# Kernel tuning notes

Hardware: AMD Instinct MI355X
Metric: run time of the kernel (lower is better)

Reference implementation:

```python
import jax, jax.numpy as jnp
import numpy as np

HEADS = 8
DIM_HEAD = 32
SCALE = DIM_HEAD ** -0.5


def setup_inputs() -> dict:
    key = jax.random.key(0)
    k1, k2, k3 = jax.random.split(key, 3)
    B, H, W, C = 16, 64, 64, 256
    hidden = HEADS * DIM_HEAD  # 256
    x = jax.random.normal(k1, (B, H, W, C), dtype=jnp.float32)
    # 1x1 convs with no bias == dense matmuls over channel dim (glorot-ish scale)
    w_qkv = jax.random.normal(k2, (C, 3 * hidden), dtype=jnp.float32) * (1.0 / np.sqrt(C))
    w_out = jax.random.normal(k3, (hidden, C), dtype=jnp.float32) * (1.0 / np.sqrt(hidden))
    return {"x": x, "w_qkv": w_qkv, "w_out": w_out}


def reference(x, w_qkv, w_out):
    B, H, W, C = x.shape
    n = H * W
    # to_qkv: 1x1 conv, no bias
    qkv = jnp.einsum('bhwc,cf->bhwf', x, w_qkv)  # [B,H,W,3*hidden]
    q, k, v = jnp.split(qkv, 3, axis=-1)

    def to_heads(t):
        # 'b x y (h c) -> b h c (x y)'
        t = t.reshape(B, n, HEADS, DIM_HEAD)
        return jnp.transpose(t, (0, 2, 3, 1))  # [B, heads, dim_head, n]

    q, k, v = to_heads(q), to_heads(k), to_heads(v)
    q = jax.nn.softmax(q, axis=-2) * SCALE      # softmax over feature dim d
    k = jax.nn.softmax(k, axis=-1)              # softmax over spatial dim n
    context = jnp.einsum('bhdn,bhen->bhde', k, v)   # [B, heads, d, e]
    out = jnp.einsum('bhde,bhdn->bhen', context, q)  # [B, heads, e, n]
    # 'b h c (x y) -> b x y (h c)'
    out = jnp.transpose(out, (0, 3, 1, 2)).reshape(B, H, W, HEADS * DIM_HEAD)
    # to_out: 1x1 conv, no bias
    return jnp.einsum('bhwf,fc->bhwc', out, w_out)
```

## Files before the change

### kernel.cpp

```cpp
#include <hip/hip_runtime.h>

using short8 = __attribute__((ext_vector_type(8))) short;
using f32x4  = __attribute__((ext_vector_type(4))) float;

#define SCALE_Q 0.17677669529663687f
#define NCHUNK 16

__device__ __forceinline__ unsigned short f2bf(float f) {
  unsigned u = __float_as_uint(f);
  return (unsigned short)((u + 0x7FFFu + ((u >> 16) & 1u)) >> 16);
}
__device__ __forceinline__ float bf2f(unsigned h) { return __uint_as_float(h << 16); }

__device__ __forceinline__ void bf8_to_f(uint4 r, float* o) {
  o[0] = bf2f(r.x & 0xffffu); o[1] = bf2f(r.x >> 16);
  o[2] = bf2f(r.y & 0xffffu); o[3] = bf2f(r.y >> 16);
  o[4] = bf2f(r.z & 0xffffu); o[5] = bf2f(r.z >> 16);
  o[6] = bf2f(r.w & 0xffffu); o[7] = bf2f(r.w >> 16);
}

__global__ __launch_bounds__(256) void prep_kernel(
    const float* __restrict__ x, const float* __restrict__ wqkv, const float* __restrict__ wout,
    unsigned short* __restrict__ xb, unsigned short* __restrict__ wqkvT,
    unsigned short* __restrict__ woutT) {
  const int blk = blockIdx.x;
  if (blk < 16384) {
    const size_t i = ((size_t)blk * 256 + threadIdx.x) * 4;
    const float4 v = *(const float4*)(x + i);
    *(ushort4*)(xb + i) = make_ushort4(f2bf(v.x), f2bf(v.y), f2bf(v.z), f2bf(v.w));
  } else if (blk < 16384 + 768) {
    const int n = blk - 16384, k = threadIdx.x;
    wqkvT[n * 256 + k] = f2bf(wqkv[(size_t)k * 768 + n]);
  } else {
    const int c = blk - 16384 - 768, f = threadIdx.x;
    woutT[c * 256 + f] = f2bf(wout[(size_t)f * 256 + c]);
  }
}

template <typename OutT, bool QSOFT, bool SWZ>
__global__ __launch_bounds__(256) void gemm_bt(
    const unsigned short* __restrict__ A, const unsigned short* __restrict__ BT,
    OutT* __restrict__ D, unsigned short* __restrict__ QS,
    int nbn, int K,
    size_t strideA, size_t strideB, size_t strideD) {
  __shared__ unsigned short As[128][40];
  __shared__ unsigned short Bs[128][40];
  int bn, bm;
  if (SWZ) {
    const int cpx = gridDim.x >> 3;
    const int lin = ((int)blockIdx.x & 7) * cpx + ((int)blockIdx.x >> 3);
    bn = lin % nbn; bm = lin / nbn;
  } else {
    bn = blockIdx.x; bm = blockIdx.y;
  }
  const int bz = blockIdx.z;
  const int tid = threadIdx.x, lane = tid & 63, wid = tid >> 6;
  const int wr = wid >> 1, wc = wid & 1;
  const int fr = lane & 15, hi = lane >> 4, fk = hi * 8;
  f32x4 acc[4][4] = {};
  const size_t abase = (size_t)bz * strideA + (size_t)bm * 128 * K;
  const size_t bbase = (size_t)bz * strideB + (size_t)bn * 128 * K;

  for (int kt = 0; kt < K; kt += 32) {
    for (int c = tid; c < 512; c += 256) {
      const int row = c >> 2, kc = (c & 3) * 8;
      *(uint4*)&As[row][kc] = *(const uint4*)(A + abase + (size_t)row * K + kt + kc);
      *(uint4*)&Bs[row][kc] = *(const uint4*)(BT + bbase + (size_t)row * K + kt + kc);
    }
    __syncthreads();
    short8 af[4], bfv[4];
#pragma unroll
    for (int i = 0; i < 4; ++i) {
      af[i]  = *(const short8*)&As[wr * 64 + i * 16 + fr][fk];
      bfv[i] = *(const short8*)&Bs[wc * 64 + i * 16 + fr][fk];
    }
#pragma unroll
    for (int mi = 0; mi < 4; ++mi)
#pragma unroll
      for (int nj = 0; nj < 4; ++nj)
        acc[mi][nj] = __builtin_amdgcn_mfma_f32_16x16x32_bf16(bfv[nj], af[mi], acc[mi][nj], 0, 0, 0);
    __syncthreads();
  }

  const size_t r0 = (size_t)bm * 128 + wr * 64;
  if (QSOFT && bn < 2) {
    const int c0 = bn * 128 + wc * 64;
#pragma unroll
    for (int mi = 0; mi < 4; ++mi) {
      const size_t row = r0 + mi * 16 + fr;
#pragma unroll
      for (int p = 0; p < 2; ++p) {
        const f32x4 a0 = acc[mi][2 * p], a1 = acc[mi][2 * p + 1];
        float mx = fmaxf(fmaxf(fmaxf(a0[0], a0[1]), fmaxf(a0[2], a0[3])),
                         fmaxf(fmaxf(a1[0], a1[1]), fmaxf(a1[2], a1[3])));
        mx = fmaxf(mx, __shfl_xor(mx, 16, 64));
        mx = fmaxf(mx, __shfl_xor(mx, 32, 64));
        float e0[4], e1[4], s = 0.f;
#pragma unroll
        for (int r = 0; r < 4; ++r) {
          e0[r] = __expf(a0[r] - mx); e1[r] = __expf(a1[r] - mx);
          s += e0[r] + e1[r];
        }
        s += __shfl_xor(s, 16, 64);
        s += __shfl_xor(s, 32, 64);
        const float inv = SCALE_Q / s;
        unsigned short* qp = QS + row * 256 + c0 + p * 32 + hi * 4;
        *(ushort4*)(qp)      = make_ushort4(f2bf(e0[0]*inv), f2bf(e0[1]*inv), f2bf(e0[2]*inv), f2bf(e0[3]*inv));
        *(ushort4*)(qp + 16) = make_ushort4(f2bf(e1[0]*inv), f2bf(e1[1]*inv), f2bf(e1[2]*inv), f2bf(e1[3]*inv));
      }
    }
    return;
  }
  const int colbase = (QSOFT ? (bn - 2) : bn) * 128 + wc * 64;
  const int ncols = QSOFT ? 512 : 256;
  OutT* Dz = D + (size_t)bz * strideD;
#pragma unroll
  for (int mi = 0; mi < 4; ++mi) {
    const size_t row = r0 + mi * 16 + fr;
#pragma unroll
    for (int nj = 0; nj < 4; ++nj) {
      const int col0 = colbase + nj * 16 + hi * 4;
      const f32x4 v = acc[mi][nj];
      if constexpr (sizeof(OutT) == 2) {
        *(ushort4*)((unsigned short*)Dz + row * ncols + col0) =
            make_ushort4(f2bf(v[0]), f2bf(v[1]), f2bf(v[2]), f2bf(v[3]));
      } else {
        *(float4*)((float*)Dz + row * ncols + col0) = make_float4(v[0], v[1], v[2], v[3]);
      }
    }
  }
}

__global__ __launch_bounds__(256) void ctx_part_kernel(const unsigned short* __restrict__ kv,
                                                       float* __restrict__ part,
                                                       float* __restrict__ spart) {
  const int blk = blockIdx.x;
  const int bh = blk >> 4, chunk = blk & 15;
  const int b = bh >> 3, h = bh & 7;
  const int tid = threadIdx.x, d = tid & 31, g = tid >> 5;
  const unsigned short* kbase =
      kv + (size_t)b * 4096 * 512 + h * 32 + (size_t)chunk * 256 * 512;
  const unsigned short* vbase = kbase + 256;

  __shared__ float ek[64][36], vv[64][36];
  float a0 = 0.f, a1 = 0.f, a2 = 0.f, a3 = 0.f, ssum = 0.f;
  const int e0 = g * 4;
  const int sn = tid >> 2, sc = (tid & 3) * 8;
  const unsigned short* kp0 = kbase + (size_t)sn * 512 + sc;
  const unsigned short* vp0 = vbase + (size_t)sn * 512 + sc;
  uint4 kr = *(const uint4*)kp0;
  uint4 vr = *(const uint4*)vp0;
  for (int n0 = 0; n0 < 256; n0 += 64) {
    float kf[8], vf[8];
    bf8_to_f(kr, kf); bf8_to_f(vr, vf);
    uint4 krn = kr, vrn = vr;
    if (n0 + 64 < 256) {
      krn = *(const uint4*)(kp0 + (size_t)(n0 + 64) * 512);
      vrn = *(const uint4*)(vp0 + (size_t)(n0 + 64) * 512);
    }
#pragma unroll
    for (int j = 0; j < 8; ++j) { ek[sn][sc + j] = __expf(kf[j]); vv[sn][sc + j] = vf[j]; }
    __syncthreads();
#pragma unroll 8
    for (int i = 0; i < 64; ++i) {
      const float kd = ek[i][d];
      const float4 v4 = *(const float4*)&vv[i][e0];
      ssum += kd;
      a0 += kd * v4.x; a1 += kd * v4.y; a2 += kd * v4.z; a3 += kd * v4.w;
    }
    __syncthreads();
    kr = krn; vr = vrn;
  }
  float* pp = part + ((size_t)chunk * 128 + bh) * 1024 + d * 32 + e0;
  pp[0] = a0; pp[1] = a1; pp[2] = a2; pp[3] = a3;
  if (g == 0) spart[((size_t)chunk * 128 + bh) * 32 + d] = ssum;
}

__global__ __launch_bounds__(256) void ctx_combine_kernel(const float* __restrict__ part,
                                                          const float* __restrict__ spart,
                                                          float* __restrict__ ctx) {
  const int bh = blockIdx.x, tid = threadIdx.x;
  __shared__ float sinv[32];
  if (tid < 32) {
    float s = 0.f;
#pragma unroll
    for (int c = 0; c < NCHUNK; ++c) s += spart[((size_t)c * 128 + bh) * 32 + tid];
    sinv[tid] = 1.0f / s;
  }
  __syncthreads();
  float4 acc = make_float4(0.f, 0.f, 0.f, 0.f);
#pragma unroll
  for (int c = 0; c < NCHUNK; ++c) {
    const float4 p = *(const float4*)(part + ((size_t)c * 128 + bh) * 1024 + tid * 4);
    acc.x += p.x; acc.y += p.y; acc.z += p.z; acc.w += p.w;
  }
  const float si = sinv[tid >> 3];
  float4* cp = (float4*)(ctx + (size_t)bh * 1024 + tid * 4);
  *cp = make_float4(acc.x * si, acc.y * si, acc.z * si, acc.w * si);
}

__global__ __launch_bounds__(256) void w2_kernel(const float* __restrict__ ctx,
                                                 const unsigned short* __restrict__ woutT,
                                                 unsigned short* __restrict__ W2T) {
  const int b = blockIdx.x >> 4, cg = blockIdx.x & 15;
  const int tid = threadIdx.x;
  __shared__ float cs[8 * 32 * 32];
  {
    const float4* src = (const float4*)(ctx + (size_t)b * 8192);
    float4* dst = (float4*)cs;
#pragma unroll
    for (int i = 0; i < 8; ++i) dst[tid + i * 256] = src[tid + i * 256];
  }
  __syncthreads();
  const int c = cg * 16 + (tid >> 4), chunk = tid & 15;
  const int h = chunk >> 1, d0 = (chunk & 1) * 16;
  float wf[32];
  {
    const uint4* wp = (const uint4*)(woutT + (size_t)c * 256 + h * 32);
    bf8_to_f(wp[0], wf + 0); bf8_to_f(wp[1], wf + 8);
    bf8_to_f(wp[2], wf + 16); bf8_to_f(wp[3], wf + 24);
  }
  unsigned short o[16];
#pragma unroll
  for (int dd = 0; dd < 16; ++dd) {
    const float* cp = cs + h * 1024 + (d0 + dd) * 32;
    float acc = 0.f;
#pragma unroll
    for (int e = 0; e < 32; ++e) acc += cp[e] * wf[e];
    o[dd] = f2bf(acc);
  }
  uint4* op = (uint4*)(W2T + ((size_t)b * 256 + c) * 256 + chunk * 16);
  op[0] = make_uint4((unsigned)o[0] | ((unsigned)o[1] << 16), (unsigned)o[2] | ((unsigned)o[3] << 16),
                     (unsigned)o[4] | ((unsigned)o[5] << 16), (unsigned)o[6] | ((unsigned)o[7] << 16));
  op[1] = make_uint4((unsigned)o[8] | ((unsigned)o[9] << 16), (unsigned)o[10] | ((unsigned)o[11] << 16),
                     (unsigned)o[12] | ((unsigned)o[13] << 16), (unsigned)o[14] | ((unsigned)o[15] << 16));
}

extern "C" void kernel_launch(void* const* d_in, const int* in_sizes, int n_in,
                              void* d_out, int out_size, void* d_ws, size_t ws_size,
                              hipStream_t stream) {
  const float* x     = (const float*)d_in[0];
  const float* wqkv  = (const float*)d_in[1];
  const float* wout  = (const float*)d_in[2];
  float* out = (float*)d_out;

  char* ws = (char*)d_ws;
  unsigned short* xb    = (unsigned short*)(ws);
  unsigned short* wqkvT = (unsigned short*)(ws + 33554432);
  unsigned short* woutT = (unsigned short*)(ws + 33947648);
  unsigned short* kv    = (unsigned short*)(ws + 34078720);
  float*          ctx   = (float*)        (ws + 101187584);
  unsigned short* qs    = (unsigned short*)(ws + 101711872);
  float*          part  = (float*)(ws);
  float*          spart = (float*)(ws + 8388608);
  unsigned short* W2T   = (unsigned short*)(ws + 12582912);

  prep_kernel<<<16384 + 768 + 256, 256, 0, stream>>>(x, wqkv, wout, xb, wqkvT, woutT);
  gemm_bt<unsigned short, true, true><<<3072, 256, 0, stream>>>(
      xb, wqkvT, kv, qs, 6, 256, 0, 0, 0);
  ctx_part_kernel<<<2048, 256, 0, stream>>>(kv, part, spart);
  ctx_combine_kernel<<<128, 256, 0, stream>>>(part, spart, ctx);
  w2_kernel<<<256, 256, 0, stream>>>(ctx, woutT, W2T);
  gemm_bt<float, false, false><<<dim3(2, 32, 16), 256, 0, stream>>>(
      qs, W2T, out, nullptr, 2, 256,
      (size_t)4096 * 256, (size_t)256 * 256, (size_t)4096 * 256);
}
```

Baseline: 166.8 us.

## Fuse fp32-to-bf16 conversion of x into QKV GEMM with register-resident B tiles

Drops the separate pass that converts x to bf16; the QKV GEMM now reads fp32 x directly and converts to bf16 while staging into shared memory. The GEMM is restructured to a 64x128 tile, with each wave keeping its full K=256 slice of B in registers and A double-buffered in LDS with a prefetch of the next stage. The aim is to avoid writing and re-reading a 32MB bf16 copy of x and to overlap global loads with MFMA work. In exchange the kernel holds more registers per thread (occupancy hint of 3 blocks) and launches twice as many blocks, each loading B from global memory.

Result: slower. 185.8 us (+11.4%).

```diff
diff --git a/kernel.cpp b/kernel.cpp
--- a/kernel.cpp
+++ b/kernel.cpp
@@ -11,6 +11,9 @@
   return (unsigned short)((u + 0x7FFFu + ((u >> 16) & 1u)) >> 16);
 }
 __device__ __forceinline__ float bf2f(unsigned h) { return __uint_as_float(h << 16); }
+__device__ __forceinline__ unsigned pack2(float a, float b) {
+  return (unsigned)f2bf(a) | ((unsigned)f2bf(b) << 16);
+}
 
 __device__ __forceinline__ void bf8_to_f(uint4 r, float* o) {
   o[0] = bf2f(r.x & 0xffffu); o[1] = bf2f(r.x >> 16);
@@ -20,105 +23,129 @@
 }
 
 __global__ __launch_bounds__(256) void prep_kernel(
-    const float* __restrict__ x, const float* __restrict__ wqkv, const float* __restrict__ wout,
-    unsigned short* __restrict__ xb, unsigned short* __restrict__ wqkvT,
-    unsigned short* __restrict__ woutT) {
+    const float* __restrict__ wqkv, const float* __restrict__ wout,
+    unsigned short* __restrict__ wqkvT, unsigned short* __restrict__ woutT) {
   const int blk = blockIdx.x;
-  if (blk < 16384) {
-    const size_t i = ((size_t)blk * 256 + threadIdx.x) * 4;
-    const float4 v = *(const float4*)(x + i);
-    *(ushort4*)(xb + i) = make_ushort4(f2bf(v.x), f2bf(v.y), f2bf(v.z), f2bf(v.w));
-  } else if (blk < 16384 + 768) {
-    const int n = blk - 16384, k = threadIdx.x;
+  if (blk < 768) {
+    const int n = blk, k = threadIdx.x;
     wqkvT[n * 256 + k] = f2bf(wqkv[(size_t)k * 768 + n]);
   } else {
-    const int c = blk - 16384 - 768, f = threadIdx.x;
+    const int c = blk - 768, f = threadIdx.x;
     woutT[c * 256 + f] = f2bf(wout[(size_t)f * 256 + c]);
   }
 }
 
-template <typename OutT, bool QSOFT, bool SWZ>
-__global__ __launch_bounds__(256) void gemm_bt(
-    const unsigned short* __restrict__ A, const unsigned short* __restrict__ BT,
+template <typename InT, typename OutT, bool QSOFT, bool SWZ>
+__global__ __launch_bounds__(256, 3) void gemm_fused(
+    const InT* __restrict__ A, const unsigned short* __restrict__ BT,
     OutT* __restrict__ D, unsigned short* __restrict__ QS,
-    int nbn, int K,
-    size_t strideA, size_t strideB, size_t strideD) {
-  __shared__ unsigned short As[128][40];
-  __shared__ unsigned short Bs[128][40];
+    int nbn, size_t strideA, size_t strideB, size_t strideD) {
+  __shared__ unsigned short As[2][64][72];
   int bn, bm;
   if (SWZ) {
     const int cpx = gridDim.x >> 3;
     const int lin = ((int)blockIdx.x & 7) * cpx + ((int)blockIdx.x >> 3);
     bn = lin % nbn; bm = lin / nbn;
   } else {
-    bn = blockIdx.x; bm = blockIdx.y;
-  }
-  const int bz = blockIdx.z;
+    bn = blockIdx.x % nbn; bm = blockIdx.x / nbn;
+  }
+  const int z = blockIdx.z;
   const int tid = threadIdx.x, lane = tid & 63, wid = tid >> 6;
-  const int wr = wid >> 1, wc = wid & 1;
-  const int fr = lane & 15, hi = lane >> 4, fk = hi * 8;
-  f32x4 acc[4][4] = {};
-  const size_t abase = (size_t)bz * strideA + (size_t)bm * 128 * K;
-  const size_t bbase = (size_t)bz * strideB + (size_t)bn * 128 * K;
-
-  for (int kt = 0; kt < K; kt += 32) {
-    for (int c = tid; c < 512; c += 256) {
-      const int row = c >> 2, kc = (c & 3) * 8;
-      *(uint4*)&As[row][kc] = *(const uint4*)(A + abase + (size_t)row * K + kt + kc);
-      *(uint4*)&Bs[row][kc] = *(const uint4*)(BT + bbase + (size_t)row * K + kt + kc);
-    }
+  const int fr = lane & 15, hi = lane >> 4;
+
+  short8 bfv[2][8];
+  {
+    const unsigned short* Bb =
+        BT + (size_t)z * strideB + ((size_t)bn * 128 + wid * 32 + fr) * 256 + hi * 8;
+#pragma unroll
+    for (int nj = 0; nj < 2; ++nj)
+#pragma unroll
+      for (int kk = 0; kk < 8; ++kk)
+        bfv[nj][kk] = *(const short8*)(Bb + (size_t)nj * 16 * 256 + kk * 32);
+  }
+
+  const int srow = tid >> 2, sk = (tid & 3) * 16;
+  const size_t arow = (size_t)bm * 64 + srow;
+
+  float4 f0, f1, f2, f3; uint4 q0, q1;
+  auto load_stage = [&](int kt) {
+    if constexpr (sizeof(InT) == 4) {
+      const float4* Ag = (const float4*)((const float*)A + (size_t)z * strideA + arow * 256 + kt + sk);
+      f0 = Ag[0]; f1 = Ag[1]; f2 = Ag[2]; f3 = Ag[3];
+    } else {
+      const unsigned short* Ag = (const unsigned short*)A + (size_t)z * strideA + arow * 256 + kt + sk;
+      q0 = *(const uint4*)Ag; q1 = *(const uint4*)(Ag + 8);
+    }
+  };
+  auto write_stage = [&](int buf) {
+    uint4 lo, hi4;
+    if constexpr (sizeof(InT) == 4) {
+      lo  = make_uint4(pack2(f0.x, f0.y), pack2(f0.z, f0.w), pack2(f1.x, f1.y), pack2(f1.z, f1.w));
+      hi4 = make_uint4(pack2(f2.x, f2.y), pack2(f2.z, f2.w), pack2(f3.x, f3.y), pack2(f3.z, f3.w));
+    } else { lo = q0; hi4 = q1; }
+    *(uint4*)&As[buf][srow][sk]     = lo;
+    *(uint4*)&As[buf][srow][sk + 8] = hi4;
+  };
+
+  f32x4 acc[4][2] = {};
+  load_stage(0); write_stage(0);
+  __syncthreads();
+  int cur = 0;
+#pragma unroll
+  for (int t = 0; t < 4; ++t) {
+    if (t < 3) load_stage((t + 1) * 64);
+#pragma unroll
+    for (int kk = 0; kk < 2; ++kk) {
+      short8 af[4];
+#pragma unroll
+      for (int mi = 0; mi < 4; ++mi)
+        af[mi] = *(const short8*)&As[cur][mi * 16 + fr][kk * 32 + hi * 8];
+#pragma unroll
+      for (int mi = 0; mi < 4; ++mi)
+#pragma unroll
+        for (int nj = 0; nj < 2; ++nj)
+          acc[mi][nj] = __builtin_amdgcn_mfma_f32_16x16x32_bf16(
+              bfv[nj][t * 2 + kk], af[mi], acc[mi][nj], 0, 0, 0);
+    }
+    if (t < 3) write_stage(cur ^ 1);
     __syncthreads();
-    short8 af[4], bfv[4];
-#pragma unroll
-    for (int i = 0; i < 4; ++i) {
-      af[i]  = *(const short8*)&As[wr * 64 + i * 16 + fr][fk];
-      bfv[i] = *(const short8*)&Bs[wc * 64 + i * 16 + fr][fk];
-    }
-#pragma unroll
-    for (int mi = 0; mi < 4; ++mi)
-#pragma unroll
-      for (int nj = 0; nj < 4; ++nj)
-        acc[mi][nj] = __builtin_amdgcn_mfma_f32_16x16x32_bf16(bfv[nj], af[mi], acc[mi][nj], 0, 0, 0);
-    __syncthreads();
-  }
-
-  const size_t r0 = (size_t)bm * 128 + wr * 64;
+    cur ^= 1;
+  }
+
+  const size_t r0 = (size_t)bm * 64;
   if (QSOFT && bn < 2) {
-    const int c0 = bn * 128 + wc * 64;
+    const int c0 = bn * 128 + wid * 32;
 #pragma unroll
     for (int mi = 0; mi < 4; ++mi) {
       const size_t row = r0 + mi * 16 + fr;
-#pragma unroll
-      for (int p = 0; p < 2; ++p) {
-        const f32x4 a0 = acc[mi][2 * p], a1 = acc[mi][2 * p + 1];
-        float mx = fmaxf(fmaxf(fmaxf(a0[0], a0[1]), fmaxf(a0[2], a0[3])),
-                         fmaxf(fmaxf(a1[0], a1[1]), fmaxf(a1[2], a1[3])));
-        mx = fmaxf(mx, __shfl_xor(mx, 16, 64));
-        mx = fmaxf(mx, __shfl_xor(mx, 32, 64));
-        float e0[4], e1[4], s = 0.f;
-#pragma unroll
-        for (int r = 0; r < 4; ++r) {
-          e0[r] = __expf(a0[r] - mx); e1[r] = __expf(a1[r] - mx);
-          s += e0[r] + e1[r];
-        }
-        s += __shfl_xor(s, 16, 64);
-        s += __shfl_xor(s, 32, 64);
-        const float inv = SCALE_Q / s;
-        unsigned short* qp = QS + row * 256 + c0 + p * 32 + hi * 4;
-        *(ushort4*)(qp)      = make_ushort4(f2bf(e0[0]*inv), f2bf(e0[1]*inv), f2bf(e0[2]*inv), f2bf(e0[3]*inv));
-        *(ushort4*)(qp + 16) = make_ushort4(f2bf(e1[0]*inv), f2bf(e1[1]*inv), f2bf(e1[2]*inv), f2bf(e1[3]*inv));
+      const f32x4 a0 = acc[mi][0], a1 = acc[mi][1];
+      float mx = fmaxf(fmaxf(fmaxf(a0[0], a0[1]), fmaxf(a0[2], a0[3])),
+                       fmaxf(fmaxf(a1[0], a1[1]), fmaxf(a1[2], a1[3])));
+      mx = fmaxf(mx, __shfl_xor(mx, 16, 64));
+      mx = fmaxf(mx, __shfl_xor(mx, 32, 64));
+      float e0[4], e1[4], s = 0.f;
+#pragma unroll
+      for (int r = 0; r < 4; ++r) {
+        e0[r] = __expf(a0[r] - mx); e1[r] = __expf(a1[r] - mx);
+        s += e0[r] + e1[r];
       }
+      s += __shfl_xor(s, 16, 64);
+      s += __shfl_xor(s, 32, 64);
+      const float inv = SCALE_Q / s;
+      unsigned short* qp = QS + row * 256 + c0 + hi * 4;
+      *(ushort4*)(qp)      = make_ushort4(f2bf(e0[0]*inv), f2bf(e0[1]*inv), f2bf(e0[2]*inv), f2bf(e0[3]*inv));
+      *(ushort4*)(qp + 16) = make_ushort4(f2bf(e1[0]*inv), f2bf(e1[1]*inv), f2bf(e1[2]*inv), f2bf(e1[3]*inv));
     }
     return;
   }
-  const int colbase = (QSOFT ? (bn - 2) : bn) * 128 + wc * 64;
+  const int colbase = (QSOFT ? (bn - 2) * 128 : bn * 128) + wid * 32;
   const int ncols = QSOFT ? 512 : 256;
-  OutT* Dz = D + (size_t)bz * strideD;
+  OutT* Dz = D + (size_t)z * strideD;
 #pragma unroll
   for (int mi = 0; mi < 4; ++mi) {
     const size_t row = r0 + mi * 16 + fr;
 #pragma unroll
-    for (int nj = 0; nj < 4; ++nj) {
+    for (int nj = 0; nj < 2; ++nj) {
       const int col0 = colbase + nj * 16 + hi * 4;
       const f32x4 v = acc[mi][nj];
       if constexpr (sizeof(OutT) == 2) {
@@ -245,23 +272,21 @@
   float* out = (float*)d_out;
 
   char* ws = (char*)d_ws;
-  unsigned short* xb    = (unsigned short*)(ws);
+  float*          part  = (float*)(ws);
+  float*          spart = (float*)(ws + 8388608);
+  unsigned short* W2T   = (unsigned short*)(ws + 12582912);
   unsigned short* wqkvT = (unsigned short*)(ws + 33554432);
   unsigned short* woutT = (unsigned short*)(ws + 33947648);
   unsigned short* kv    = (unsigned short*)(ws + 34078720);
   float*          ctx   = (float*)        (ws + 101187584);
   unsigned short* qs    = (unsigned short*)(ws + 101711872);
-  float*          part  = (float*)(ws);
-  float*          spart = (float*)(ws + 8388608);
-  unsigned short* W2T   = (unsigned short*)(ws + 12582912);
-
-  prep_kernel<<<16384 + 768 + 256, 256, 0, stream>>>(x, wqkv, wout, xb, wqkvT, woutT);
-  gemm_bt<unsigned short, true, true><<<3072, 256, 0, stream>>>(
-      xb, wqkvT, kv, qs, 6, 256, 0, 0, 0);
+
+  prep_kernel<<<1024, 256, 0, stream>>>(wqkv, wout, wqkvT, woutT);
+  gemm_fused<float, unsigned short, true, true><<<6144, 256, 0, stream>>>(
+      x, wqkvT, kv, qs, 6, 0, 0, 0);
   ctx_part_kernel<<<2048, 256, 0, stream>>>(kv, part, spart);
   ctx_combine_kernel<<<128, 256, 0, stream>>>(part, spart, ctx);
   w2_kernel<<<256, 256, 0, stream>>>(ctx, woutT, W2T);
-  gemm_bt<float, false, false><<<dim3(2, 32, 16), 256, 0, stream>>>(
-      qs, W2T, out, nullptr, 2, 256,
-      (size_t)4096 * 256, (size_t)256 * 256, (size_t)4096 * 256);
-}
+  gemm_fused<unsigned short, float, false, false><<<dim3(128, 1, 16), 256, 0, stream>>>(
+      qs, W2T, out, nullptr, 2, (size_t)4096 * 256, (size_t)256 * 256, (size_t)4096 * 256);
+}
```

## Fuse x bf16 conversion into QKV GEMM load and exp(k) into epilogue

Applied to the files above, without the earlier changes.

The QKV GEMM now reads fp32 x directly and converts it to bf16 while staging into shared memory. This drops the separate pass that wrote a bf16 copy of x. The exponential of k moves from ctx_part_kernel into the GEMM epilogue for the k columns, and the XCD-aware block swizzle is replaced by a plain 2D grid. The GEMM now reads twice the A bytes per tile and may lose L2 locality without the swizzle; exp(k) is stored in bf16 rather than computed in fp32.

Result: slower. 181.5 us (+8.8%).

```diff
diff --git a/kernel.cpp b/kernel.cpp
--- a/kernel.cpp
+++ b/kernel.cpp
@@ -11,6 +11,9 @@
   return (unsigned short)((u + 0x7FFFu + ((u >> 16) & 1u)) >> 16);
 }
 __device__ __forceinline__ float bf2f(unsigned h) { return __uint_as_float(h << 16); }
+__device__ __forceinline__ unsigned pack2(float a, float b) {
+  return (unsigned)f2bf(a) | ((unsigned)f2bf(b) << 16);
+}
 
 __device__ __forceinline__ void bf8_to_f(uint4 r, float* o) {
   o[0] = bf2f(r.x & 0xffffu); o[1] = bf2f(r.x >> 16);
@@ -20,40 +23,26 @@
 }
 
 __global__ __launch_bounds__(256) void prep_kernel(
-    const float* __restrict__ x, const float* __restrict__ wqkv, const float* __restrict__ wout,
-    unsigned short* __restrict__ xb, unsigned short* __restrict__ wqkvT,
-    unsigned short* __restrict__ woutT) {
+    const float* __restrict__ wqkv, const float* __restrict__ wout,
+    unsigned short* __restrict__ wqkvT, unsigned short* __restrict__ woutT) {
   const int blk = blockIdx.x;
-  if (blk < 16384) {
-    const size_t i = ((size_t)blk * 256 + threadIdx.x) * 4;
-    const float4 v = *(const float4*)(x + i);
-    *(ushort4*)(xb + i) = make_ushort4(f2bf(v.x), f2bf(v.y), f2bf(v.z), f2bf(v.w));
-  } else if (blk < 16384 + 768) {
-    const int n = blk - 16384, k = threadIdx.x;
+  if (blk < 768) {
+    const int n = blk, k = threadIdx.x;
     wqkvT[n * 256 + k] = f2bf(wqkv[(size_t)k * 768 + n]);
   } else {
-    const int c = blk - 16384 - 768, f = threadIdx.x;
+    const int c = blk - 768, f = threadIdx.x;
     woutT[c * 256 + f] = f2bf(wout[(size_t)f * 256 + c]);
   }
 }
 
-template <typename OutT, bool QSOFT, bool SWZ>
+template <typename InT, typename OutT, bool QSOFT>
 __global__ __launch_bounds__(256) void gemm_bt(
-    const unsigned short* __restrict__ A, const unsigned short* __restrict__ BT,
+    const InT* __restrict__ A, const unsigned short* __restrict__ BT,
     OutT* __restrict__ D, unsigned short* __restrict__ QS,
-    int nbn, int K,
-    size_t strideA, size_t strideB, size_t strideD) {
+    int K, size_t strideA, size_t strideB, size_t strideD) {
   __shared__ unsigned short As[128][40];
   __shared__ unsigned short Bs[128][40];
-  int bn, bm;
-  if (SWZ) {
-    const int cpx = gridDim.x >> 3;
-    const int lin = ((int)blockIdx.x & 7) * cpx + ((int)blockIdx.x >> 3);
-    bn = lin % nbn; bm = lin / nbn;
-  } else {
-    bn = blockIdx.x; bm = blockIdx.y;
-  }
-  const int bz = blockIdx.z;
+  const int bn = blockIdx.x, bm = blockIdx.y, bz = blockIdx.z;
   const int tid = threadIdx.x, lane = tid & 63, wid = tid >> 6;
   const int wr = wid >> 1, wc = wid & 1;
   const int fr = lane & 15, hi = lane >> 4, fk = hi * 8;
@@ -64,7 +53,15 @@
   for (int kt = 0; kt < K; kt += 32) {
     for (int c = tid; c < 512; c += 256) {
       const int row = c >> 2, kc = (c & 3) * 8;
-      *(uint4*)&As[row][kc] = *(const uint4*)(A + abase + (size_t)row * K + kt + kc);
+      if constexpr (sizeof(InT) == 4) {
+        const float* Ap = (const float*)A + abase + (size_t)row * K + kt + kc;
+        const float4 u = *(const float4*)Ap, w = *(const float4*)(Ap + 4);
+        *(uint4*)&As[row][kc] =
+            make_uint4(pack2(u.x, u.y), pack2(u.z, u.w), pack2(w.x, w.y), pack2(w.z, w.w));
+      } else {
+        *(uint4*)&As[row][kc] =
+            *(const uint4*)((const unsigned short*)A + abase + (size_t)row * K + kt + kc);
+      }
       *(uint4*)&Bs[row][kc] = *(const uint4*)(BT + bbase + (size_t)row * K + kt + kc);
     }
     __syncthreads();
@@ -113,6 +110,7 @@
   }
   const int colbase = (QSOFT ? (bn - 2) : bn) * 128 + wc * 64;
   const int ncols = QSOFT ? 512 : 256;
+  const bool EXPK = QSOFT && (bn < 4);
   OutT* Dz = D + (size_t)bz * strideD;
 #pragma unroll
   for (int mi = 0; mi < 4; ++mi) {
@@ -120,7 +118,11 @@
 #pragma unroll
     for (int nj = 0; nj < 4; ++nj) {
       const int col0 = colbase + nj * 16 + hi * 4;
-      const f32x4 v = acc[mi][nj];
+      f32x4 v = acc[mi][nj];
+      if (EXPK) {
+#pragma unroll
+        for (int r = 0; r < 4; ++r) v[r] = __expf(v[r]);
+      }
       if constexpr (sizeof(OutT) == 2) {
         *(ushort4*)((unsigned short*)Dz + row * ncols + col0) =
             make_ushort4(f2bf(v[0]), f2bf(v[1]), f2bf(v[2]), f2bf(v[3]));
@@ -159,7 +161,7 @@
       vrn = *(const uint4*)(vp0 + (size_t)(n0 + 64) * 512);
     }
 #pragma unroll
-    for (int j = 0; j < 8; ++j) { ek[sn][sc + j] = __expf(kf[j]); vv[sn][sc + j] = vf[j]; }
+    for (int j = 0; j < 8; ++j) { ek[sn][sc + j] = kf[j]; vv[sn][sc + j] = vf[j]; }
     __syncthreads();
 #pragma unroll 8
     for (int i = 0; i < 64; ++i) {
@@ -245,23 +247,22 @@
   float* out = (float*)d_out;
 
   char* ws = (char*)d_ws;
-  unsigned short* xb    = (unsigned short*)(ws);
+  float*          part  = (float*)(ws);
+  float*          spart = (float*)(ws + 8388608);
+  unsigned short* W2T   = (unsigned short*)(ws + 12582912);
   unsigned short* wqkvT = (unsigned short*)(ws + 33554432);
   unsigned short* woutT = (unsigned short*)(ws + 33947648);
   unsigned short* kv    = (unsigned short*)(ws + 34078720);
   float*          ctx   = (float*)        (ws + 101187584);
   unsigned short* qs    = (unsigned short*)(ws + 101711872);
-  float*          part  = (float*)(ws);
-  float*          spart = (float*)(ws + 8388608);
-  unsigned short* W2T   = (unsigned short*)(ws + 12582912);
-
-  prep_kernel<<<16384 + 768 + 256, 256, 0, stream>>>(x, wqkv, wout, xb, wqkvT, woutT);
-  gemm_bt<unsigned short, true, true><<<3072, 256, 0, stream>>>(
-      xb, wqkvT, kv, qs, 6, 256, 0, 0, 0);
+
+  prep_kernel<<<1024, 256, 0, stream>>>(wqkv, wout, wqkvT, woutT);
+  gemm_bt<float, unsigned short, true><<<dim3(6, 512, 1), 256, 0, stream>>>(
+      x, wqkvT, kv, qs, 256, 0, 0, 0);
   ctx_part_kernel<<<2048, 256, 0, stream>>>(kv, part, spart);
   ctx_combine_kernel<<<128, 256, 0, stream>>>(part, spart, ctx);
   w2_kernel<<<256, 256, 0, stream>>>(ctx, woutT, W2T);
-  gemm_bt<float, false, false><<<dim3(2, 32, 16), 256, 0, stream>>>(
-      qs, W2T, out, nullptr, 2, 256,
+  gemm_bt<unsigned short, float, false><<<dim3(2, 32, 16), 256, 0, stream>>>(
+      qs, W2T, out, nullptr, 256,
       (size_t)4096 * 256, (size_t)256 * 256, (size_t)4096 * 256);
 }
```
